# Performance work log

Hardware: AMD Instinct MI355X
Metric: run time of the kernel (lower is better)

The kernel has to match this reference:

```python
import jax, jax.numpy as jnp
import numpy as np

R, C, CH, BA = 2048, 1024, 8, 8
EPS = 1e-10


def setup_inputs() -> dict:
    key = jax.random.key(0)
    k1, k2, k3 = jax.random.split(key, 3)
    # kaiming_uniform_ on [R, CH*BA]: fan_in = CH*BA, bound = sqrt(6/fan_in)
    bound = float(np.sqrt(6.0 / (CH * BA)))
    W = jax.random.uniform(k1, (R, CH * BA), jnp.float32, -bound, bound)
    D = (jax.random.uniform(k2, (R, C)) < 0.1).astype(jnp.float32)
    # Gumbel(0,1) noise, replicating the torch quirk: -log(eps - log(u + eps))
    u = jax.random.uniform(k3, (R, CH * BA), jnp.float32)
    g = -jnp.log(EPS - jnp.log(u + EPS))
    return {"W": W, "D": D, "g": g, "i": 100}


def reference(W, D, g, i):
    # temp = 1000 - 999/3999*i is computed in torch but GumbelSoftmax.forward
    # ignores it and always uses temperature=1, so i has no effect on the math.
    P = jax.nn.softmax(W + g, axis=-1).reshape(R, CH, BA)        # [R,CH,BA]
    x = P[:, None, :, :] * D[:, :, None, None]                    # [R,C,CH,BA]

    nnz_ch_ba = jnp.sum(x, axis=(0, 1))                           # [CH,BA]
    max_nnz_ch = jnp.max(nnz_ch_ba, axis=-1)                      # [CH] (torch dim=2 on 2D -> last axis)

    col_ch = 1.0 - jnp.prod(jnp.prod(1.0 - x, axis=0), axis=2)    # [C,CH]
    num_col_ch = jnp.sum(col_ch, axis=0)                          # [CH]
    num_row_ch = jnp.sum(P, axis=(0, 2))                          # [CH]

    col_density_ch = jnp.sum(
        jnp.sum(x, axis=(0, 3)) / num_row_ch / num_col_ch, axis=0)  # [CH]

    tot_ch = max_nnz_ch + num_col_ch + num_row_ch                 # [CH]

    num_row_sel = jnp.sum(
        (jnp.max(P.reshape(R, -1), axis=1) > 0.99).astype(jnp.float32))
    return (P, tot_ch, max_nnz_ch, num_col_ch, num_row_ch,
            nnz_ch_ba, col_density_ch, num_row_sel)
```

## Files before the change

kernel.cpp:

```cpp
#include <hip/hip_runtime.h>
#include <math.h>

#define R 2048
#define C 1024
#define CH 8
#define K 64

#define OFF_P     0
#define OFF_TOT   (R*K)
#define OFF_MAX   (OFF_TOT + 8)
#define OFF_NCOL  (OFF_MAX + 8)
#define OFF_NROW  (OFF_NCOL + 8)
#define OFF_NNZ   (OFF_NROW + 8)
#define OFF_DEN   (OFF_NNZ + 64)
#define OFF_SEL   (OFF_DEN + 8)

#define WS_CP   0
#define WS_NP   131072
#define WS_NR   (WS_NP + 16384)
#define WS_SEL  (WS_NR + 128)

__global__ __launch_bounds__(512) void k1(
    const float* __restrict__ W, const float* __restrict__ Dm,
    const float* __restrict__ g, float* __restrict__ P,
    float* __restrict__ ws)
{
    const int tid  = threadIdx.x;
    const int lane = tid & 63;
    const int w    = tid >> 6;
    const int rc   = blockIdx.x >> 4;
    const int cb   = blockIdx.x & 15;
    const int row0 = rc * 128 + w * 16;
    const int col  = cb * 64 + lane;

    __shared__ float partp[8][8][64];
    __shared__ float rn[8][64];
    __shared__ float rp[8][8];
    __shared__ float rsel[8];

    float pr[8] = {1.f,1.f,1.f,1.f,1.f,1.f,1.f,1.f};
    float nnz_l = 0.f, acc_srow = 0.f, acc_sel = 0.f;

    #pragma unroll 4
    for (int i = 0; i < 16; ++i) {
        const int row = row0 + i;
        float d = Dm[(size_t)row * C + col];

        float z = W[row * K + lane] + g[row * K + lane];
        float m = z;
        #pragma unroll
        for (int off = 32; off >= 1; off >>= 1)
            m = fmaxf(m, __shfl_xor(m, off, 64));
        float e = __expf(z - m);
        float s = e;
        #pragma unroll
        for (int off = 32; off >= 1; off >>= 1)
            s += __shfl_xor(s, off, 64);
        float p = e * __builtin_amdgcn_rcpf(s);
        if (cb == 0) P[row * K + lane] = p;

        float om = 1.0f - p, sc = p;
        #pragma unroll
        for (int off = 1; off <= 4; off <<= 1) {
            om *= __shfl_xor(om, off, 64);
            sc += __shfl_xor(sc, off, 64);
        }
        if ((lane & 7) == 0) acc_srow += sc;

        if (cb == 0) {
            float pm = p;
            #pragma unroll
            for (int off = 32; off >= 1; off >>= 1)
                pm = fmaxf(pm, __shfl_xor(pm, off, 64));
            if (lane == 0 && pm > 0.99f) acc_sel += 1.0f;
        }

        float ds = d;
        #pragma unroll
        for (int off = 32; off >= 1; off >>= 1)
            ds += __shfl_xor(ds, off, 64);
        nnz_l += ds * p;

        float q0 = __shfl(om,  0, 64), q1 = __shfl(om,  8, 64);
        float q2 = __shfl(om, 16, 64), q3 = __shfl(om, 24, 64);
        float q4 = __shfl(om, 32, 64), q5 = __shfl(om, 40, 64);
        float q6 = __shfl(om, 48, 64), q7 = __shfl(om, 56, 64);
        pr[0] *= fmaf(d, q0 - 1.f, 1.f);
        pr[1] *= fmaf(d, q1 - 1.f, 1.f);
        pr[2] *= fmaf(d, q2 - 1.f, 1.f);
        pr[3] *= fmaf(d, q3 - 1.f, 1.f);
        pr[4] *= fmaf(d, q4 - 1.f, 1.f);
        pr[5] *= fmaf(d, q5 - 1.f, 1.f);
        pr[6] *= fmaf(d, q6 - 1.f, 1.f);
        pr[7] *= fmaf(d, q7 - 1.f, 1.f);
    }

    #pragma unroll
    for (int ch = 0; ch < 8; ++ch) partp[w][ch][lane] = pr[ch];
    rn[w][lane] = nnz_l;
    if ((lane & 7) == 0) rp[w][lane >> 3] = acc_srow;
    if (lane == 0) rsel[w] = acc_sel;
    __syncthreads();

    {
        const int cl = tid & 63, ch = tid >> 6;
        float v = partp[0][ch][cl] * partp[1][ch][cl]
                * partp[2][ch][cl] * partp[3][ch][cl]
                * partp[4][ch][cl] * partp[5][ch][cl]
                * partp[6][ch][cl] * partp[7][ch][cl];
        ws[WS_CP + rc * 8192 + ch * 1024 + cb * 64 + cl] = v;
    }
    if (w == 0) {
        float v = rn[0][lane] + rn[1][lane] + rn[2][lane] + rn[3][lane]
                + rn[4][lane] + rn[5][lane] + rn[6][lane] + rn[7][lane];
        ws[WS_NP + blockIdx.x * 64 + lane] = v;
    }
    if (cb == 0 && tid < 8) {
        float v = 0.f;
        #pragma unroll
        for (int ww = 0; ww < 8; ++ww) v += rp[ww][tid];
        ws[WS_NR + rc * 8 + tid] = v;
    }
    if (cb == 0 && tid == 0) {
        float v = 0.f;
        #pragma unroll
        for (int ww = 0; ww < 8; ++ww) v += rsel[ww];
        ws[WS_SEL + rc] = v;
    }
}

__global__ __launch_bounds__(1024) void k2(const float* __restrict__ ws,
                                           float* __restrict__ out)
{
    const int tid = threadIdx.x;
    __shared__ float red[1024];
    __shared__ float np[8][64];
    __shared__ float nc8[8], nr8[8];

    {
        const int ch = tid >> 7;
        const int c0 = tid & 127;
        float ncl = 0.f;
        #pragma unroll
        for (int j = 0; j < 8; ++j) {
            const float* base = ws + WS_CP + ch * 1024 + j * 128 + c0;
            float prod = base[0];
            #pragma unroll
            for (int rc = 1; rc < 16; ++rc) prod *= base[rc * 8192];
            ncl += 1.0f - prod;
        }
        red[tid] = ncl;
    }

    if (tid < 512) {
        const int l = tid & 63, h = tid >> 6;
        const float* b = ws + WS_NP + h * 32 * 64 + l;
        float v = 0.f;
        #pragma unroll
        for (int bb = 0; bb < 32; ++bb) v += b[bb * 64];
        np[h][l] = v;
    }
    if (tid >= 512 && tid < 520) {
        const int ch = tid - 512;
        float v = 0.f;
        #pragma unroll
        for (int rc = 0; rc < 16; ++rc) v += ws[WS_NR + rc * 8 + ch];
        nr8[ch] = v;
    }
    if (tid == 520) {
        float v = 0.f;
        #pragma unroll
        for (int rc = 0; rc < 16; ++rc) v += ws[WS_SEL + rc];
        out[OFF_SEL] = v;
    }
    __syncthreads();

    #pragma unroll
    for (int off = 64; off >= 1; off >>= 1) {
        if ((tid & 127) < off) red[tid] += red[tid + off];
        __syncthreads();
    }
    if ((tid & 127) == 0) nc8[tid >> 7] = red[tid];
    __syncthreads();

    if (tid < 64) {
        float nnzv = np[0][tid] + np[1][tid] + np[2][tid] + np[3][tid]
                   + np[4][tid] + np[5][tid] + np[6][tid] + np[7][tid];
        out[OFF_NNZ + tid] = nnzv;
        float sum = nnzv, mx = nnzv;
        #pragma unroll
        for (int off = 1; off <= 4; off <<= 1) {
            sum += __shfl_xor(sum, off, 64);
            mx = fmaxf(mx, __shfl_xor(mx, off, 64));
        }
        if ((tid & 7) == 0) {
            const int ch = tid >> 3;
            const float nr = nr8[ch], nc = nc8[ch];
            out[OFF_TOT  + ch] = mx + nc + nr;
            out[OFF_MAX  + ch] = mx;
            out[OFF_NCOL + ch] = nc;
            out[OFF_NROW + ch] = nr;
            out[OFF_DEN  + ch] = sum / nr / nc;
        }
    }
}

extern "C" void kernel_launch(void* const* d_in, const int* in_sizes, int n_in,
                              void* d_out, int out_size, void* d_ws, size_t ws_size,
                              hipStream_t stream) {
    const float* W = (const float*)d_in[0];
    const float* D = (const float*)d_in[1];
    const float* g = (const float*)d_in[2];
    float* out = (float*)d_out;
    float* ws  = (float*)d_ws;

    k1<<<256, 512, 0, stream>>>(W, D, g, out, ws);
    k2<<<1,  1024, 0, stream>>>(ws, out);
}
```

Measured before the change: 91.79 us.

## Compute column products as log-sums and split softmax from column accumulation

The per-column product of (1 - p) terms is replaced by a sum of log2 values. A new first kernel computes each row's softmax once and writes per-row channel log-values, row sums and nnz partials. A second kernel multiplies D by those log-values and accumulates per-column sums with atomicAdd. A final kernel exponentiates and reduces. This removes the softmax and shuffle work that the old layout repeated across 16 column blocks. In exchange it reads D twice, adds a third launch and global atomics, and log-domain accumulation can lose precision for p near 1.

```diff
diff --git a/kernel.cpp b/kernel.cpp
--- a/kernel.cpp
+++ b/kernel.cpp
@@ -15,10 +15,11 @@
 #define OFF_DEN   (OFF_NNZ + 64)
 #define OFF_SEL   (OFF_DEN + 8)
 
-#define WS_CP   0
-#define WS_NP   131072
-#define WS_NR   (WS_NP + 16384)
-#define WS_SEL  (WS_NR + 128)
+#define WS_LQ   0
+#define WS_COL  16384
+#define WS_NP   24576
+#define WS_NR   40960
+#define WS_SEL  43008
 
 __global__ __launch_bounds__(512) void k1(
     const float* __restrict__ W, const float* __restrict__ Dm,
@@ -28,150 +29,144 @@
     const int tid  = threadIdx.x;
     const int lane = tid & 63;
     const int w    = tid >> 6;
-    const int rc   = blockIdx.x >> 4;
-    const int cb   = blockIdx.x & 15;
-    const int row0 = rc * 128 + w * 16;
-    const int col  = cb * 64 + lane;
-
-    __shared__ float partp[8][8][64];
+    const int row  = blockIdx.x * 8 + w;
+
+    if (tid < 32) ws[WS_COL + blockIdx.x * 32 + tid] = 0.0f;
+
+    float z = W[row * K + lane] + g[row * K + lane];
+    float m = z;
+    #pragma unroll
+    for (int off = 32; off >= 1; off >>= 1)
+        m = fmaxf(m, __shfl_xor(m, off, 64));
+    float e = __expf(z - m);
+    float s = e;
+    #pragma unroll
+    for (int off = 32; off >= 1; off >>= 1)
+        s += __shfl_xor(s, off, 64);
+    float p = e * __builtin_amdgcn_rcpf(s);
+    P[row * K + lane] = p;
+
+    const float4* Drow = (const float4*)(Dm + (size_t)row * C);
+    float ds = 0.0f;
+    #pragma unroll
+    for (int j = 0; j < 4; ++j) {
+        float4 v = Drow[lane + 64 * j];
+        ds += (v.x + v.y) + (v.z + v.w);
+    }
+    #pragma unroll
+    for (int off = 32; off >= 1; off >>= 1)
+        ds += __shfl_xor(ds, off, 64);
+
+    float om = 1.0f - p, sc = p;
+    #pragma unroll
+    for (int off = 1; off <= 4; off <<= 1) {
+        om *= __shfl_xor(om, off, 64);
+        sc += __shfl_xor(sc, off, 64);
+    }
+    if ((lane & 7) == 0)
+        ws[WS_LQ + row * CH + (lane >> 3)] =
+            fmaxf(__builtin_amdgcn_logf(om), -1.0e30f);
+
+    float pm = p;
+    #pragma unroll
+    for (int off = 32; off >= 1; off >>= 1)
+        pm = fmaxf(pm, __shfl_xor(pm, off, 64));
+
     __shared__ float rn[8][64];
     __shared__ float rp[8][8];
     __shared__ float rsel[8];
-
-    float pr[8] = {1.f,1.f,1.f,1.f,1.f,1.f,1.f,1.f};
-    float nnz_l = 0.f, acc_srow = 0.f, acc_sel = 0.f;
-
+    rn[w][lane] = p * ds;
+    if ((lane & 7) == 0) rp[w][lane >> 3] = sc;
+    if (lane == 0) rsel[w] = (pm > 0.99f) ? 1.0f : 0.0f;
+    __syncthreads();
+
+    if (tid < 64) {
+        float v = rn[0][tid] + rn[1][tid] + rn[2][tid] + rn[3][tid]
+                + rn[4][tid] + rn[5][tid] + rn[6][tid] + rn[7][tid];
+        ws[WS_NP + blockIdx.x * 64 + tid] = v;
+    }
+    if (tid < 8) {
+        float v = 0.0f;
+        #pragma unroll
+        for (int ww = 0; ww < 8; ++ww) v += rp[ww][tid];
+        ws[WS_NR + blockIdx.x * 8 + tid] = v;
+    }
+    if (tid == 0) {
+        float v = 0.0f;
+        #pragma unroll
+        for (int ww = 0; ww < 8; ++ww) v += rsel[ww];
+        ws[WS_SEL + blockIdx.x] = v;
+    }
+}
+
+__global__ __launch_bounds__(256) void k2(
+    const float* __restrict__ Dm, float* __restrict__ ws)
+{
+    const int tid = threadIdx.x;
+    const int ct  = blockIdx.x & 3;
+    const int rc  = blockIdx.x >> 2;
+    const int col = ct * 256 + tid;
+
+    float l0=0,l1=0,l2=0,l3=0,l4=0,l5=0,l6=0,l7=0;
+    const int r0 = rc * 32;
     #pragma unroll 4
-    for (int i = 0; i < 16; ++i) {
-        const int row = row0 + i;
-        float d = Dm[(size_t)row * C + col];
-
-        float z = W[row * K + lane] + g[row * K + lane];
-        float m = z;
-        #pragma unroll
-        for (int off = 32; off >= 1; off >>= 1)
-            m = fmaxf(m, __shfl_xor(m, off, 64));
-        float e = __expf(z - m);
-        float s = e;
-        #pragma unroll
-        for (int off = 32; off >= 1; off >>= 1)
-            s += __shfl_xor(s, off, 64);
-        float p = e * __builtin_amdgcn_rcpf(s);
-        if (cb == 0) P[row * K + lane] = p;
-
-        float om = 1.0f - p, sc = p;
-        #pragma unroll
-        for (int off = 1; off <= 4; off <<= 1) {
-            om *= __shfl_xor(om, off, 64);
-            sc += __shfl_xor(sc, off, 64);
-        }
-        if ((lane & 7) == 0) acc_srow += sc;
-
-        if (cb == 0) {
-            float pm = p;
-            #pragma unroll
-            for (int off = 32; off >= 1; off >>= 1)
-                pm = fmaxf(pm, __shfl_xor(pm, off, 64));
-            if (lane == 0 && pm > 0.99f) acc_sel += 1.0f;
-        }
-
-        float ds = d;
-        #pragma unroll
-        for (int off = 32; off >= 1; off >>= 1)
-            ds += __shfl_xor(ds, off, 64);
-        nnz_l += ds * p;
-
-        float q0 = __shfl(om,  0, 64), q1 = __shfl(om,  8, 64);
-        float q2 = __shfl(om, 16, 64), q3 = __shfl(om, 24, 64);
-        float q4 = __shfl(om, 32, 64), q5 = __shfl(om, 40, 64);
-        float q6 = __shfl(om, 48, 64), q7 = __shfl(om, 56, 64);
-        pr[0] *= fmaf(d, q0 - 1.f, 1.f);
-        pr[1] *= fmaf(d, q1 - 1.f, 1.f);
-        pr[2] *= fmaf(d, q2 - 1.f, 1.f);
-        pr[3] *= fmaf(d, q3 - 1.f, 1.f);
-        pr[4] *= fmaf(d, q4 - 1.f, 1.f);
-        pr[5] *= fmaf(d, q5 - 1.f, 1.f);
-        pr[6] *= fmaf(d, q6 - 1.f, 1.f);
-        pr[7] *= fmaf(d, q7 - 1.f, 1.f);
-    }
-
-    #pragma unroll
-    for (int ch = 0; ch < 8; ++ch) partp[w][ch][lane] = pr[ch];
-    rn[w][lane] = nnz_l;
-    if ((lane & 7) == 0) rp[w][lane >> 3] = acc_srow;
-    if (lane == 0) rsel[w] = acc_sel;
-    __syncthreads();
-
-    {
-        const int cl = tid & 63, ch = tid >> 6;
-        float v = partp[0][ch][cl] * partp[1][ch][cl]
-                * partp[2][ch][cl] * partp[3][ch][cl]
-                * partp[4][ch][cl] * partp[5][ch][cl]
-                * partp[6][ch][cl] * partp[7][ch][cl];
-        ws[WS_CP + rc * 8192 + ch * 1024 + cb * 64 + cl] = v;
-    }
-    if (w == 0) {
-        float v = rn[0][lane] + rn[1][lane] + rn[2][lane] + rn[3][lane]
-                + rn[4][lane] + rn[5][lane] + rn[6][lane] + rn[7][lane];
-        ws[WS_NP + blockIdx.x * 64 + lane] = v;
-    }
-    if (cb == 0 && tid < 8) {
-        float v = 0.f;
-        #pragma unroll
-        for (int ww = 0; ww < 8; ++ww) v += rp[ww][tid];
-        ws[WS_NR + rc * 8 + tid] = v;
-    }
-    if (cb == 0 && tid == 0) {
-        float v = 0.f;
-        #pragma unroll
-        for (int ww = 0; ww < 8; ++ww) v += rsel[ww];
-        ws[WS_SEL + rc] = v;
-    }
-}
-
-__global__ __launch_bounds__(1024) void k2(const float* __restrict__ ws,
+    for (int i = 0; i < 32; ++i) {
+        const int r = r0 + i;
+        float d = Dm[(size_t)r * C + col];
+        const float* lr = ws + WS_LQ + r * CH;
+        l0 += d * lr[0]; l1 += d * lr[1]; l2 += d * lr[2]; l3 += d * lr[3];
+        l4 += d * lr[4]; l5 += d * lr[5]; l6 += d * lr[6]; l7 += d * lr[7];
+    }
+    float* ca = ws + WS_COL;
+    atomicAdd(&ca[0 * 1024 + col], l0);
+    atomicAdd(&ca[1 * 1024 + col], l1);
+    atomicAdd(&ca[2 * 1024 + col], l2);
+    atomicAdd(&ca[3 * 1024 + col], l3);
+    atomicAdd(&ca[4 * 1024 + col], l4);
+    atomicAdd(&ca[5 * 1024 + col], l5);
+    atomicAdd(&ca[6 * 1024 + col], l6);
+    atomicAdd(&ca[7 * 1024 + col], l7);
+}
+
+__global__ __launch_bounds__(1024) void k3(const float* __restrict__ ws,
                                            float* __restrict__ out)
 {
     const int tid = threadIdx.x;
     __shared__ float red[1024];
-    __shared__ float np[8][64];
-    __shared__ float nc8[8], nr8[8];
+    __shared__ float npr[16][64];
+    __shared__ float nrr[8][8];
+    __shared__ float selr[64];
+    __shared__ float nc8[8];
 
     {
-        const int ch = tid >> 7;
-        const int c0 = tid & 127;
-        float ncl = 0.f;
-        #pragma unroll
-        for (int j = 0; j < 8; ++j) {
-            const float* base = ws + WS_CP + ch * 1024 + j * 128 + c0;
-            float prod = base[0];
-            #pragma unroll
-            for (int rc = 1; rc < 16; ++rc) prod *= base[rc * 8192];
-            ncl += 1.0f - prod;
-        }
+        const int ch = tid >> 7, c0 = tid & 127;
+        float ncl = 0.0f;
+        #pragma unroll
+        for (int j = 0; j < 8; ++j)
+            ncl += 1.0f - __builtin_amdgcn_exp2f(
+                              ws[WS_COL + ch * 1024 + j * 128 + c0]);
         red[tid] = ncl;
     }
-
-    if (tid < 512) {
-        const int l = tid & 63, h = tid >> 6;
-        const float* b = ws + WS_NP + h * 32 * 64 + l;
-        float v = 0.f;
-        #pragma unroll
-        for (int bb = 0; bb < 32; ++bb) v += b[bb * 64];
-        np[h][l] = v;
-    }
-    if (tid >= 512 && tid < 520) {
-        const int ch = tid - 512;
-        float v = 0.f;
-        #pragma unroll
-        for (int rc = 0; rc < 16; ++rc) v += ws[WS_NR + rc * 8 + ch];
-        nr8[ch] = v;
-    }
-    if (tid == 520) {
-        float v = 0.f;
-        #pragma unroll
-        for (int rc = 0; rc < 16; ++rc) v += ws[WS_SEL + rc];
-        out[OFF_SEL] = v;
+    {
+        const int l = tid & 63, grp = tid >> 6;
+        float v = 0.0f;
+        #pragma unroll
+        for (int b = 0; b < 16; ++b)
+            v += ws[WS_NP + (grp * 16 + b) * 64 + l];
+        npr[grp][l] = v;
+    }
+    if (tid < 64) {
+        const int ch = tid & 7, grp = tid >> 3;
+        float v = 0.0f;
+        #pragma unroll
+        for (int b = 0; b < 32; ++b)
+            v += ws[WS_NR + (grp * 32 + b) * CH + ch];
+        nrr[grp][ch] = v;
+        float sv = 0.0f;
+        #pragma unroll
+        for (int j = 0; j < 4; ++j)
+            sv += ws[WS_SEL + j * 64 + tid];
+        selr[tid] = sv;
     }
     __syncthreads();
 
@@ -184,18 +179,29 @@
     __syncthreads();
 
     if (tid < 64) {
-        float nnzv = np[0][tid] + np[1][tid] + np[2][tid] + np[3][tid]
-                   + np[4][tid] + np[5][tid] + np[6][tid] + np[7][tid];
+        float nnzv = 0.0f;
+        #pragma unroll
+        for (int g2 = 0; g2 < 16; ++g2) nnzv += npr[g2][tid];
         out[OFF_NNZ + tid] = nnzv;
+
         float sum = nnzv, mx = nnzv;
         #pragma unroll
         for (int off = 1; off <= 4; off <<= 1) {
             sum += __shfl_xor(sum, off, 64);
             mx = fmaxf(mx, __shfl_xor(mx, off, 64));
         }
+        float sv = selr[tid];
+        #pragma unroll
+        for (int off = 32; off >= 1; off >>= 1)
+            sv += __shfl_xor(sv, off, 64);
+        if (tid == 0) out[OFF_SEL] = sv;
+
         if ((tid & 7) == 0) {
             const int ch = tid >> 3;
-            const float nr = nr8[ch], nc = nc8[ch];
+            float nr = 0.0f;
+            #pragma unroll
+            for (int g2 = 0; g2 < 8; ++g2) nr += nrr[g2][ch];
+            const float nc = nc8[ch];
             out[OFF_TOT  + ch] = mx + nc + nr;
             out[OFF_MAX  + ch] = mx;
             out[OFF_NCOL + ch] = nc;
@@ -215,5 +221,6 @@
     float* ws  = (float*)d_ws;
 
     k1<<<256, 512, 0, stream>>>(W, D, g, out, ws);
-    k2<<<1,  1024, 0, stream>>>(ws, out);
-}
+    k2<<<256, 256, 0, stream>>>(D, ws);
+    k3<<<1,  1024, 0, stream>>>(ws, out);
+}
```

Measured after the change: 77.13 us. 1.19x faster.
